# Optimization experiments

Hardware: AMD Instinct MI355X
Metric: run time of the kernel (lower is better)

The kernel has to match this reference:

```python
import jax, jax.numpy as jnp
import numpy as np

B, P, ED, AD, DD, E, V, T = 64, 196, 2048, 512, 512, 300, 1000, 96


def setup_inputs() -> dict:
    key = jax.random.key(0)
    ks = jax.random.split(key, 24)
    s = 0.02  # small init scale for weights
    lens = jax.random.randint(ks[2], (B,), 2, T + 1).astype(jnp.int32)
    lens = lens.at[0].set(T)  # ensure max(decode_lengths) == T-1 (static)
    return {
        'encoder_out': jax.random.normal(ks[0], (B, P, ED), jnp.float32),
        'encoded_captions': jax.random.randint(ks[1], (B, T), 0, V),
        'caption_lengths': lens,
        'emb': jax.random.uniform(ks[3], (V, E), jnp.float32, -0.1, 0.1),
        'W_enc_att': jax.random.normal(ks[4], (ED, AD), jnp.float32) * s,
        'b_enc_att': jnp.zeros((AD,), jnp.float32),
        'W_dec_att': jax.random.normal(ks[5], (DD, AD), jnp.float32) * s,
        'b_dec_att': jnp.zeros((AD,), jnp.float32),
        'w_full': jax.random.normal(ks[6], (AD,), jnp.float32) * s,
        'b_full': jnp.zeros((), jnp.float32),
        'W_init_h': jax.random.normal(ks[7], (ED, DD), jnp.float32) * s,
        'b_init_h': jnp.zeros((DD,), jnp.float32),
        'W_init_c': jax.random.normal(ks[8], (ED, DD), jnp.float32) * s,
        'b_init_c': jnp.zeros((DD,), jnp.float32),
        'W_fbeta': jax.random.normal(ks[9], (DD, ED), jnp.float32) * s,
        'b_fbeta': jnp.zeros((ED,), jnp.float32),
        'W_ih': jax.random.normal(ks[10], (E + ED, 4 * DD), jnp.float32) * s,
        'b_ih': jnp.zeros((4 * DD,), jnp.float32),
        'W_hh': jax.random.normal(ks[11], (DD, 4 * DD), jnp.float32) * s,
        'b_hh': jnp.zeros((4 * DD,), jnp.float32),
        'W_fc': jax.random.uniform(ks[12], (DD, V), jnp.float32, -0.1, 0.1),
        'b_fc': jnp.zeros((V,), jnp.float32),
    }


def reference(encoder_out, encoded_captions, caption_lengths, emb,
              W_enc_att, b_enc_att, W_dec_att, b_dec_att, w_full, b_full,
              W_init_h, b_init_h, W_init_c, b_init_c, W_fbeta, b_fbeta,
              W_ih, b_ih, W_hh, b_hh, W_fc, b_fc):
    # Sort by caption length, descending (stable like torch.sort on ints)
    sort_ind = jnp.argsort(-caption_lengths)
    lens = caption_lengths[sort_ind]
    eo = encoder_out[sort_ind]                  # [B,P,ED]
    caps = encoded_captions[sort_ind]           # [B,T]
    decode_lengths = lens - 1                   # [B]

    embs = emb[caps]                            # [B,T,E]
    mean_eo = eo.mean(axis=1)                   # [B,ED]
    h0 = mean_eo @ W_init_h + b_init_h          # [B,DD]
    c0 = mean_eo @ W_init_c + b_init_c

    # encoder-side attention projection is step-invariant: hoist it
    att1 = eo @ W_enc_att + b_enc_att           # [B,P,AD]

    Tdec = T - 1
    ts = jnp.arange(Tdec)
    masks = (decode_lengths[None, :] > ts[:, None]).astype(eo.dtype)  # [Tdec,B]
    emb_seq = jnp.swapaxes(embs[:, :Tdec, :], 0, 1)                    # [Tdec,B,E]

    def step(carry, xs):
        h, c = carry
        emb_t, m = xs                           # [B,E], [B]
        mb = m[:, None]
        # Bahdanau attention
        att2 = h @ W_dec_att + b_dec_att        # [B,AD]
        e = jnp.einsum('bpa,a->bp', jax.nn.relu(att1 + att2[:, None, :]), w_full) + b_full
        alpha = jax.nn.softmax(e, axis=1)       # [B,P]
        awe = jnp.einsum('bpd,bp->bd', eo, alpha)  # [B,ED]
        gate = jax.nn.sigmoid(h @ W_fbeta + b_fbeta)
        x = jnp.concatenate([emb_t, gate * awe], axis=1)  # [B,E+ED]
        # LSTMCell (torch gate order: i, f, g, o)
        gates = x @ W_ih + b_ih + h @ W_hh + b_hh
        i, f, g, o = jnp.split(gates, 4, axis=1)
        c_new = jax.nn.sigmoid(f) * c + jax.nn.sigmoid(i) * jnp.tanh(g)
        h_new = jax.nn.sigmoid(o) * jnp.tanh(c_new)
        # only active rows (sorted so they are a prefix) update state
        h2 = mb * h_new + (1.0 - mb) * h
        c2 = mb * c_new + (1.0 - mb) * c
        preds = (h2 @ W_fc + b_fc) * mb         # dropout = identity (eval)
        return (h2, c2), (preds, alpha * mb)

    (_, _), (preds, alphas) = jax.lax.scan(step, (h0, c0), (emb_seq, masks))
    predictions = jnp.swapaxes(preds, 0, 1)     # [B,Tdec,V]
    alphas = jnp.swapaxes(alphas, 0, 1)         # [B,Tdec,P]
    return predictions, caps, decode_lengths, alphas, sort_ind
```

## Files before the change

kernel.cpp:

```cpp
#include <hip/hip_runtime.h>
#include <stddef.h>
#include <math.h>

static constexpr int B = 64, P = 196, ED = 2048, AD = 512, DD = 512, E = 300, V = 1000, T = 96, TD = 95;
static constexpr int KX = E + ED;
static constexpr int KTOT = KX + DD;
static constexpr int KSPLIT = 8;
static constexpr int KPER = 368;
static constexpr int NG = 4 * DD;

static constexpr size_t POFF   = 0;
static constexpr size_t CAPOFF = (size_t)B * TD * V;
static constexpr size_t DLOFF  = CAPOFF + (size_t)B * T;
static constexpr size_t AOFF   = DLOFF + B;
static constexpr size_t SOFF   = AOFF + (size_t)B * TD * P;

__device__ __forceinline__ float sigm(float x) { return 1.0f / (1.0f + expf(-x)); }

__global__ __launch_bounds__(64) void k_sort(const int* __restrict__ lens,
                                             const int* __restrict__ caps_in,
                                             int* __restrict__ sidx,
                                             int* __restrict__ dlen,
                                             int* __restrict__ caps_s,
                                             float* __restrict__ out) {
    __shared__ int sl[B];
    __shared__ int ss[B];
    int i = threadIdx.x;
    sl[i] = lens[i];
    __syncthreads();
    int li = sl[i];
    int r = 0;
    for (int j = 0; j < B; j++) {
        int lj = sl[j];
        r += (lj > li) || (lj == li && j < i);
    }
    ss[r] = i;
    sidx[r] = i;
    dlen[r] = li - 1;
    out[DLOFF + r] = (float)(li - 1);
    out[SOFF + r] = (float)i;
    __syncthreads();
    for (int idx = i; idx < B * T; idx += B) {
        int b = idx / T, tt = idx % T;
        int v = caps_in[ss[b] * T + tt];
        caps_s[idx] = v;
        out[CAPOFF + idx] = (float)v;
    }
}

__global__ __launch_bounds__(256) void k_mean(const float* __restrict__ eo,
                                              const int* __restrict__ sidx,
                                              float* __restrict__ mean_eo) {
    int b = blockIdx.y;
    int d = blockIdx.x * 256 + threadIdx.x;
    const float* base = eo + ((size_t)sidx[b] * P) * ED + d;
    float s = 0.f;
    for (int p = 0; p < P; p++) s += base[(size_t)p * ED];
    mean_eo[(size_t)b * ED + d] = s * (1.0f / (float)P);
}

__global__ __launch_bounds__(256) void k_init(const float* __restrict__ mean_eo,
                                              const float* __restrict__ Wh, const float* __restrict__ bh,
                                              const float* __restrict__ Wc, const float* __restrict__ bc,
                                              float* __restrict__ h0, float* __restrict__ c0,
                                              float* __restrict__ xT) {
    int idx = blockIdx.x * 256 + threadIdx.x;
    int b = idx >> 9, j = idx & 511;
    const float* m = mean_eo + (size_t)b * ED;
    float ah = bh[j], ac = bc[j];
    for (int k = 0; k < ED; k++) {
        float mv = m[k];
        ah += mv * Wh[(size_t)k * DD + j];
        ac += mv * Wc[(size_t)k * DD + j];
    }
    h0[idx] = ah;
    c0[idx] = ac;
    xT[(size_t)(KX + j) * B + b] = ah;
}

__global__ __launch_bounds__(256) void k_att1(const float* __restrict__ eo,
                                              const float* __restrict__ W,
                                              const float* __restrict__ bias,
                                              const int* __restrict__ sidx,
                                              float* __restrict__ att1) {
    int m0 = blockIdx.x * 64, n0 = blockIdx.y * 64;
    __shared__ float sA[16][68];
    __shared__ float sB[16][68];
    int tid = threadIdx.x;
    int tx = tid & 15, ty = tid >> 4;
    float acc[4][4] = {};

    int la_m = tid >> 2;
    int la_k = (tid & 3) * 4;
    int lb_k = tid >> 4;
    int lb_n = (tid & 15) * 4;

    int mA = m0 + la_m;
    int bA = mA / P, pA = mA % P;
    const float* arow = eo + ((size_t)sidx[bA] * P + pA) * ED;

    for (int k0 = 0; k0 < ED; k0 += 16) {
        float4 av = *(const float4*)(arow + k0 + la_k);
        sA[la_k + 0][la_m] = av.x;
        sA[la_k + 1][la_m] = av.y;
        sA[la_k + 2][la_m] = av.z;
        sA[la_k + 3][la_m] = av.w;
        float4 bv = *(const float4*)(W + (size_t)(k0 + lb_k) * AD + n0 + lb_n);
        *(float4*)&sB[lb_k][lb_n] = bv;
        __syncthreads();
#pragma unroll
        for (int kk = 0; kk < 16; kk++) {
            float4 a4 = *(const float4*)&sA[kk][ty * 4];
            float4 b4 = *(const float4*)&sB[kk][tx * 4];
            float av_[4] = {a4.x, a4.y, a4.z, a4.w};
            float bv_[4] = {b4.x, b4.y, b4.z, b4.w};
#pragma unroll
            for (int i = 0; i < 4; i++)
#pragma unroll
                for (int j = 0; j < 4; j++) acc[i][j] += av_[i] * bv_[j];
        }
        __syncthreads();
    }
#pragma unroll
    for (int i = 0; i < 4; i++) {
        int m = m0 + ty * 4 + i;
        int n = n0 + tx * 4;
        float4 o;
        o.x = acc[i][0] + bias[n + 0];
        o.y = acc[i][1] + bias[n + 1];
        o.z = acc[i][2] + bias[n + 2];
        o.w = acc[i][3] + bias[n + 3];
        *(float4*)(att1 + (size_t)m * AD + n) = o;
    }
}

__global__ __launch_bounds__(256) void kA1(const float* __restrict__ hprev,
                                           const float* __restrict__ Wda, const float* __restrict__ bda,
                                           const float* __restrict__ Wfb, const float* __restrict__ bfb,
                                           const float* __restrict__ emb,
                                           const int* __restrict__ caps_s,
                                           float* __restrict__ att2g,
                                           float* __restrict__ fg,
                                           float* __restrict__ xT, int t) {
    int bx = blockIdx.x;
    int tid = threadIdx.x;
    if (bx >= 80) {
        int k0 = (bx - 80) * 60;
        for (int l = tid; l < 60 * 64; l += 256) {
            int r = l >> 6, b = l & 63;
            int k = k0 + r;
            int cap = caps_s[b * T + t];
            xT[(size_t)k * B + b] = emb[(size_t)cap * E + k];
        }
        return;
    }
    int n0 = bx * 32;
    bool is_att = (n0 < AD);
    __shared__ float sH[16][68];
    __shared__ float sW[16][36];
    float acc[4][2] = {};
    int tb = tid & 15, tn = tid >> 4;

    for (int k0 = 0; k0 < DD; k0 += 16) {
        {
            int b = tid >> 2, q = tid & 3;
            float4 hv = *(const float4*)(hprev + (size_t)b * DD + k0 + q * 4);
            sH[q * 4 + 0][b] = hv.x;
            sH[q * 4 + 1][b] = hv.y;
            sH[q * 4 + 2][b] = hv.z;
            sH[q * 4 + 3][b] = hv.w;
        }
        if (tid < 128) {
            int kk = tid >> 3, nn = (tid & 7) * 4;
            float4 wv;
            if (is_att) wv = *(const float4*)(Wda + (size_t)(k0 + kk) * AD + n0 + nn);
            else        wv = *(const float4*)(Wfb + (size_t)(k0 + kk) * ED + (n0 - AD) + nn);
            *(float4*)&sW[kk][nn] = wv;
        }
        __syncthreads();
#pragma unroll
        for (int kk = 0; kk < 16; kk++) {
            float4 hv = *(const float4*)&sH[kk][tb * 4];
            float w0 = sW[kk][tn * 2 + 0];
            float w1 = sW[kk][tn * 2 + 1];
            acc[0][0] += hv.x * w0; acc[0][1] += hv.x * w1;
            acc[1][0] += hv.y * w0; acc[1][1] += hv.y * w1;
            acc[2][0] += hv.z * w0; acc[2][1] += hv.z * w1;
            acc[3][0] += hv.w * w0; acc[3][1] += hv.w * w1;
        }
        __syncthreads();
    }
#pragma unroll
    for (int i = 0; i < 4; i++)
#pragma unroll
        for (int j = 0; j < 2; j++) {
            int b = tb * 4 + i;
            int n = n0 + tn * 2 + j;
            float v = acc[i][j];
            if (is_att) att2g[(size_t)b * AD + n] = v + bda[n];
            else {
                int d = n - AD;
                fg[(size_t)b * ED + d] = sigm(v + bfb[d]);
            }
        }
}

__global__ __launch_bounds__(1024) void kA2(const float* __restrict__ att2g,
                                            const float* __restrict__ att1,
                                            const float* __restrict__ wf,
                                            const float* __restrict__ bfv,
                                            const int* __restrict__ dlen,
                                            float* __restrict__ alpha,
                                            float* __restrict__ out, int t) {
    int b = blockIdx.x;
    int tid = threadIdx.x;
    __shared__ float sa2[AD];
    __shared__ float swf[AD];
    __shared__ float se[P];
    __shared__ float red[1024];

    if (tid < AD) {
        sa2[tid] = att2g[(size_t)b * AD + tid];
        swf[tid] = wf[tid];
    }
    __syncthreads();

    int w = tid >> 6, lane = tid & 63;
    float bf0 = bfv[0];
#pragma unroll 2
    for (int p = w; p < P; p += 16) {
        const float* row = att1 + ((size_t)b * P + p) * AD + lane * 8;
        float4 u0 = *(const float4*)row;
        float4 u1 = *(const float4*)(row + 4);
        float4 s0 = *(const float4*)&sa2[lane * 8];
        float4 s1 = *(const float4*)&sa2[lane * 8 + 4];
        float4 w0 = *(const float4*)&swf[lane * 8];
        float4 w1 = *(const float4*)&swf[lane * 8 + 4];
        float acc = fmaxf(u0.x + s0.x, 0.f) * w0.x + fmaxf(u0.y + s0.y, 0.f) * w0.y +
                    fmaxf(u0.z + s0.z, 0.f) * w0.z + fmaxf(u0.w + s0.w, 0.f) * w0.w +
                    fmaxf(u1.x + s1.x, 0.f) * w1.x + fmaxf(u1.y + s1.y, 0.f) * w1.y +
                    fmaxf(u1.z + s1.z, 0.f) * w1.z + fmaxf(u1.w + s1.w, 0.f) * w1.w;
#pragma unroll
        for (int m = 32; m >= 1; m >>= 1) acc += __shfl_xor(acc, m, 64);
        if (lane == 0) se[p] = acc + bf0;
    }
    __syncthreads();

    red[tid] = (tid < P) ? se[tid] : -1e30f;
    __syncthreads();
    for (int s = 512; s > 0; s >>= 1) {
        if (tid < s) red[tid] = fmaxf(red[tid], red[tid + s]);
        __syncthreads();
    }
    float mx = red[0];
    __syncthreads();
    float ex = (tid < P) ? expf(se[tid] - mx) : 0.f;
    red[tid] = ex;
    __syncthreads();
    for (int s = 512; s > 0; s >>= 1) {
        if (tid < s) red[tid] += red[tid + s];
        __syncthreads();
    }
    float inv = 1.0f / red[0];
    if (tid < P) {
        float a = ex * inv;
        alpha[(size_t)b * P + tid] = a;
        float m = (dlen[b] > t) ? 1.f : 0.f;
        out[AOFF + ((size_t)b * TD + t) * P + tid] = a * m;
    }
}

__global__ __launch_bounds__(256) void kB(const float* __restrict__ eo,
                                          const int* __restrict__ sidx,
                                          const float* __restrict__ alpha,
                                          const float* __restrict__ fg,
                                          float* __restrict__ xT) {
    int b = blockIdx.y, ch = blockIdx.x, tid = threadIdx.x;
    int pg = tid >> 6, lane = tid & 63;
    __shared__ float sal[P];
    __shared__ float part[4][260];
    if (tid < P) sal[tid] = alpha[(size_t)b * P + tid];
    __syncthreads();
    int d = ch * 256 + lane * 4;
    const float* base = eo + ((size_t)sidx[b] * P) * ED + d;
    float ax = 0.f, ay = 0.f, az = 0.f, aw = 0.f;
#pragma unroll 7
    for (int i = 0; i < 49; i++) {
        int p = pg + i * 4;
        float4 v = *(const float4*)(base + (size_t)p * ED);
        float a = sal[p];
        ax += v.x * a; ay += v.y * a; az += v.z * a; aw += v.w * a;
    }
    part[pg][lane * 4 + 0] = ax;
    part[pg][lane * 4 + 1] = ay;
    part[pg][lane * 4 + 2] = az;
    part[pg][lane * 4 + 3] = aw;
    __syncthreads();
    if (tid < 64) {
        int d0 = ch * 256 + tid * 4;
        float4 g = *(const float4*)(fg + (size_t)b * ED + d0);
        float s0 = part[0][tid * 4 + 0] + part[1][tid * 4 + 0] + part[2][tid * 4 + 0] + part[3][tid * 4 + 0];
        float s1 = part[0][tid * 4 + 1] + part[1][tid * 4 + 1] + part[2][tid * 4 + 1] + part[3][tid * 4 + 1];
        float s2 = part[0][tid * 4 + 2] + part[1][tid * 4 + 2] + part[2][tid * 4 + 2] + part[3][tid * 4 + 2];
        float s3 = part[0][tid * 4 + 3] + part[1][tid * 4 + 3] + part[2][tid * 4 + 3] + part[3][tid * 4 + 3];
        xT[(size_t)(E + d0 + 0) * B + b] = g.x * s0;
        xT[(size_t)(E + d0 + 1) * B + b] = g.y * s1;
        xT[(size_t)(E + d0 + 2) * B + b] = g.z * s2;
        xT[(size_t)(E + d0 + 3) * B + b] = g.w * s3;
    }
}

__global__ __launch_bounds__(256) void kC(const float* __restrict__ xT,
                                          const float* __restrict__ Wih,
                                          const float* __restrict__ Whh,
                                          float* __restrict__ part) {
    int bx = blockIdx.x;
    int ks = bx >> 6, nb = bx & 63;
    int n0 = nb * 32;
    int tid = threadIdx.x;
    int tb = tid & 15, tn = tid >> 4;
    __shared__ float sW[16][36];
    float acc[4][2] = {};
    int kbase = ks * KPER;

    for (int tile = 0; tile < 23; tile++) {
        int k0 = kbase + tile * 16;
        if (tid < 128) {
            int kk = tid >> 3, nn = (tid & 7) * 4;
            int kg = k0 + kk;
            float4 wv = make_float4(0.f, 0.f, 0.f, 0.f);
            if (kg < KX) wv = *(const float4*)&Wih[(size_t)kg * NG + n0 + nn];
            else if (kg < KTOT) wv = *(const float4*)&Whh[(size_t)(kg - KX) * NG + n0 + nn];
            *(float4*)&sW[kk][nn] = wv;
        }
        __syncthreads();
#pragma unroll
        for (int kk = 0; kk < 16; kk++) {
            int kg = k0 + kk;
            float4 xv = make_float4(0.f, 0.f, 0.f, 0.f);
            if (kg < KTOT) xv = *(const float4*)&xT[(size_t)kg * B + tb * 4];
            float w0 = sW[kk][tn * 2 + 0];
            float w1 = sW[kk][tn * 2 + 1];
            acc[0][0] += xv.x * w0; acc[0][1] += xv.x * w1;
            acc[1][0] += xv.y * w0; acc[1][1] += xv.y * w1;
            acc[2][0] += xv.z * w0; acc[2][1] += xv.z * w1;
            acc[3][0] += xv.w * w0; acc[3][1] += xv.w * w1;
        }
        __syncthreads();
    }
    float* pr = part + (size_t)ks * B * NG;
#pragma unroll
    for (int i = 0; i < 4; i++)
#pragma unroll
        for (int j = 0; j < 2; j++) {
            int b = tb * 4 + i, n = n0 + tn * 2 + j;
            pr[(size_t)b * NG + n] = acc[i][j];
        }
}

__global__ __launch_bounds__(256) void kD(const float* __restrict__ part,
                                          const float* __restrict__ bih,
                                          const float* __restrict__ bhh,
                                          const float* __restrict__ hprev,
                                          const float* __restrict__ cc,
                                          const int* __restrict__ dlen,
                                          float* __restrict__ hseq_t,
                                          float* __restrict__ cn,
                                          float* __restrict__ xT, int t) {
    int idx = blockIdx.x * 256 + threadIdx.x;
    int b = idx >> 9, j = idx & 511;
    float gi = bih[j] + bhh[j];
    float gf = bih[DD + j] + bhh[DD + j];
    float gg = bih[2 * DD + j] + bhh[2 * DD + j];
    float go = bih[3 * DD + j] + bhh[3 * DD + j];
#pragma unroll
    for (int s = 0; s < KSPLIT; s++) {
        const float* pr = part + ((size_t)s * B + b) * NG;
        gi += pr[j];
        gf += pr[DD + j];
        gg += pr[2 * DD + j];
        go += pr[3 * DD + j];
    }
    float cold = cc[idx], hold = hprev[idx];
    float cnew = sigm(gf) * cold + sigm(gi) * tanhf(gg);
    float hnew = sigm(go) * tanhf(cnew);
    bool m = dlen[b] > t;
    float h2 = m ? hnew : hold;
    float c2 = m ? cnew : cold;
    hseq_t[idx] = h2;
    cn[idx] = c2;
    xT[(size_t)(KX + j) * B + b] = h2;
}

__global__ __launch_bounds__(256) void k_predsall(const float* __restrict__ hseq,
                                                  const float* __restrict__ Wfc,
                                                  const float* __restrict__ bfc,
                                                  const int* __restrict__ dlen,
                                                  float* __restrict__ out) {
    int t = blockIdx.x;
    int n0 = blockIdx.y * 64;
    int tid = threadIdx.x;
    int tx = tid & 15, ty = tid >> 4;
    __shared__ float sA[16][68];
    __shared__ float sB[16][68];
    float acc[4][4] = {};
    const float* A = hseq + (size_t)t * B * DD;

    for (int k0 = 0; k0 < DD; k0 += 16) {
        {
            int b = tid >> 2, q = tid & 3;
            float4 hv = *(const float4*)(A + (size_t)b * DD + k0 + q * 4);
            sA[q * 4 + 0][b] = hv.x;
            sA[q * 4 + 1][b] = hv.y;
            sA[q * 4 + 2][b] = hv.z;
            sA[q * 4 + 3][b] = hv.w;
        }
        {
            int kk = tid >> 4, nn = (tid & 15) * 4;
            int c = n0 + nn;
            const float* wrow = Wfc + (size_t)(k0 + kk) * V;
            float4 wv;
            if (c + 3 < V) wv = *(const float4*)(wrow + c);
            else {
                wv.x = (c + 0 < V) ? wrow[c + 0] : 0.f;
                wv.y = (c + 1 < V) ? wrow[c + 1] : 0.f;
                wv.z = (c + 2 < V) ? wrow[c + 2] : 0.f;
                wv.w = (c + 3 < V) ? wrow[c + 3] : 0.f;
            }
            *(float4*)&sB[kk][nn] = wv;
        }
        __syncthreads();
#pragma unroll
        for (int kk = 0; kk < 16; kk++) {
            float4 a4 = *(const float4*)&sA[kk][ty * 4];
            float4 b4 = *(const float4*)&sB[kk][tx * 4];
            float av_[4] = {a4.x, a4.y, a4.z, a4.w};
            float bv_[4] = {b4.x, b4.y, b4.z, b4.w};
#pragma unroll
            for (int i = 0; i < 4; i++)
#pragma unroll
                for (int j = 0; j < 4; j++) acc[i][j] += av_[i] * bv_[j];
        }
        __syncthreads();
    }
#pragma unroll
    for (int i = 0; i < 4; i++) {
        int b = ty * 4 + i;
        bool m = dlen[b] > t;
#pragma unroll
        for (int j = 0; j < 4; j++) {
            int n = n0 + tx * 4 + j;
            if (n < V)
                out[POFF + ((size_t)b * TD + t) * V + n] = m ? (acc[i][j] + bfc[n]) : 0.f;
        }
    }
}

extern "C" void kernel_launch(void* const* d_in, const int* in_sizes, int n_in,
                              void* d_out, int out_size, void* d_ws, size_t ws_size,
                              hipStream_t stream) {
    const float* eo    = (const float*)d_in[0];
    const int*   caps  = (const int*)d_in[1];
    const int*   lens  = (const int*)d_in[2];
    const float* emb   = (const float*)d_in[3];
    const float* Wea   = (const float*)d_in[4];
    const float* bea   = (const float*)d_in[5];
    const float* Wda   = (const float*)d_in[6];
    const float* bda   = (const float*)d_in[7];
    const float* wfull = (const float*)d_in[8];
    const float* bfull = (const float*)d_in[9];
    const float* Wih_  = (const float*)d_in[10];
    const float* bih_  = (const float*)d_in[11];
    const float* Wic   = (const float*)d_in[12];
    const float* bic   = (const float*)d_in[13];
    const float* Wfb   = (const float*)d_in[14];
    const float* bfb   = (const float*)d_in[15];
    const float* Wih   = (const float*)d_in[16];
    const float* bih   = (const float*)d_in[17];
    const float* Whh   = (const float*)d_in[18];
    const float* bhh   = (const float*)d_in[19];
    const float* Wfc   = (const float*)d_in[20];
    const float* bfc   = (const float*)d_in[21];
    float* out = (float*)d_out;

    char* w = (char*)d_ws;
    auto carve = [&](size_t bytes) -> void* {
        void* p = (void*)w;
        w += (bytes + 255) & ~(size_t)255;
        return p;
    };
    int* sidx      = (int*)carve(B * 4);
    int* dlen      = (int*)carve(B * 4);
    int* caps_s    = (int*)carve((size_t)B * T * 4);
    float* mean_eo = (float*)carve((size_t)B * ED * 4);
    float* h0      = (float*)carve((size_t)B * DD * 4);
    float* cb0     = (float*)carve((size_t)B * DD * 4);
    float* cb1     = (float*)carve((size_t)B * DD * 4);
    float* att1    = (float*)carve((size_t)B * P * AD * 4);
    float* alphaW  = (float*)carve((size_t)B * P * 4);
    float* att2g   = (float*)carve((size_t)B * AD * 4);
    float* fg      = (float*)carve((size_t)B * ED * 4);
    float* xT      = (float*)carve((size_t)KTOT * B * 4);
    float* part    = (float*)carve((size_t)KSPLIT * B * NG * 4);
    float* hseq    = (float*)carve((size_t)TD * B * DD * 4);
    float* cb[2] = {cb0, cb1};

    k_sort<<<1, 64, 0, stream>>>(lens, caps, sidx, dlen, caps_s, out);
    k_mean<<<dim3(ED / 256, B), 256, 0, stream>>>(eo, sidx, mean_eo);
    k_init<<<(B * DD) / 256, 256, 0, stream>>>(mean_eo, Wih_, bih_, Wic, bic, h0, cb0, xT);
    k_att1<<<dim3((B * P) / 64, AD / 64), 256, 0, stream>>>(eo, Wea, bea, sidx, att1);

    for (int t = 0; t < TD; t++) {
        const float* hprev = (t == 0) ? h0 : (hseq + (size_t)(t - 1) * B * DD);
        float* cc = cb[t & 1];
        float* cn = cb[(t + 1) & 1];
        kA1<<<85, 256, 0, stream>>>(hprev, Wda, bda, Wfb, bfb, emb, caps_s, att2g, fg, xT, t);
        kA2<<<64, 1024, 0, stream>>>(att2g, att1, wfull, bfull, dlen, alphaW, out, t);
        kB<<<dim3(8, B), 256, 0, stream>>>(eo, sidx, alphaW, fg, xT);
        kC<<<512, 256, 0, stream>>>(xT, Wih, Whh, part);
        kD<<<(B * DD) / 256, 256, 0, stream>>>(part, bih, bhh, hprev, cc, dlen,
                                               hseq + (size_t)t * B * DD, cn, xT, t);
    }
    k_predsall<<<dim3(TD, 16), 256, 0, stream>>>(hseq, Wfc, bfc, dlen, out);
}
```

Measured before the change: 17.75 ms.

## Fuse LSTM cell update and attention projection into per-step kernels, precompute embeddings

Result: slower. 19.30 ms (+8.7%).

```diff
diff --git a/kernel.cpp b/kernel.cpp
--- a/kernel.cpp
+++ b/kernel.cpp
@@ -45,6 +45,19 @@
         int v = caps_in[ss[b] * T + tt];
         caps_s[idx] = v;
         out[CAPOFF + idx] = (float)v;
+    }
+}
+
+__global__ __launch_bounds__(256) void k_emball(const float* __restrict__ emb,
+                                                const int* __restrict__ caps_s,
+                                                float* __restrict__ embT) {
+    int t = blockIdx.x;
+    int k0 = blockIdx.y * 60;
+    for (int l = threadIdx.x; l < 60 * 64; l += 256) {
+        int r = l >> 6, b = l & 63;
+        int k = k0 + r;
+        int cap = caps_s[b * T + t];
+        embT[((size_t)t * E + k) * B + b] = emb[(size_t)cap * E + k];
     }
 }
 
@@ -134,95 +147,77 @@
     }
 }
 
-__global__ __launch_bounds__(256) void kA1(const float* __restrict__ hprev,
-                                           const float* __restrict__ Wda, const float* __restrict__ bda,
-                                           const float* __restrict__ Wfb, const float* __restrict__ bfb,
-                                           const float* __restrict__ emb,
-                                           const int* __restrict__ caps_s,
-                                           float* __restrict__ att2g,
-                                           float* __restrict__ fg,
-                                           float* __restrict__ xT, int t) {
-    int bx = blockIdx.x;
-    int tid = threadIdx.x;
-    if (bx >= 80) {
-        int k0 = (bx - 80) * 60;
-        for (int l = tid; l < 60 * 64; l += 256) {
-            int r = l >> 6, b = l & 63;
-            int k = k0 + r;
-            int cap = caps_s[b * T + t];
-            xT[(size_t)k * B + b] = emb[(size_t)cap * E + k];
-        }
-        return;
-    }
-    int n0 = bx * 32;
-    bool is_att = (n0 < AD);
-    __shared__ float sH[16][68];
-    __shared__ float sW[16][36];
-    float acc[4][2] = {};
-    int tb = tid & 15, tn = tid >> 4;
-
-    for (int k0 = 0; k0 < DD; k0 += 16) {
-        {
-            int b = tid >> 2, q = tid & 3;
-            float4 hv = *(const float4*)(hprev + (size_t)b * DD + k0 + q * 4);
-            sH[q * 4 + 0][b] = hv.x;
-            sH[q * 4 + 1][b] = hv.y;
-            sH[q * 4 + 2][b] = hv.z;
-            sH[q * 4 + 3][b] = hv.w;
-        }
-        if (tid < 128) {
-            int kk = tid >> 3, nn = (tid & 7) * 4;
-            float4 wv;
-            if (is_att) wv = *(const float4*)(Wda + (size_t)(k0 + kk) * AD + n0 + nn);
-            else        wv = *(const float4*)(Wfb + (size_t)(k0 + kk) * ED + (n0 - AD) + nn);
-            *(float4*)&sW[kk][nn] = wv;
-        }
-        __syncthreads();
-#pragma unroll
-        for (int kk = 0; kk < 16; kk++) {
-            float4 hv = *(const float4*)&sH[kk][tb * 4];
-            float w0 = sW[kk][tn * 2 + 0];
-            float w1 = sW[kk][tn * 2 + 1];
-            acc[0][0] += hv.x * w0; acc[0][1] += hv.x * w1;
-            acc[1][0] += hv.y * w0; acc[1][1] += hv.y * w1;
-            acc[2][0] += hv.z * w0; acc[2][1] += hv.z * w1;
-            acc[3][0] += hv.w * w0; acc[3][1] += hv.w * w1;
-        }
-        __syncthreads();
-    }
-#pragma unroll
-    for (int i = 0; i < 4; i++)
-#pragma unroll
-        for (int j = 0; j < 2; j++) {
-            int b = tb * 4 + i;
-            int n = n0 + tn * 2 + j;
-            float v = acc[i][j];
-            if (is_att) att2g[(size_t)b * AD + n] = v + bda[n];
-            else {
-                int d = n - AD;
-                fg[(size_t)b * ED + d] = sigm(v + bfb[d]);
-            }
-        }
-}
-
-__global__ __launch_bounds__(1024) void kA2(const float* __restrict__ att2g,
-                                            const float* __restrict__ att1,
-                                            const float* __restrict__ wf,
-                                            const float* __restrict__ bfv,
-                                            const int* __restrict__ dlen,
-                                            float* __restrict__ alpha,
-                                            float* __restrict__ out, int t) {
+__global__ __launch_bounds__(1024) void kA2f(const float* __restrict__ part,
+                                             const float* __restrict__ bih,
+                                             const float* __restrict__ bhh,
+                                             const float* __restrict__ h0,
+                                             const float* __restrict__ cread,
+                                             float* __restrict__ cwrite,
+                                             const float* __restrict__ Wda,
+                                             const float* __restrict__ bda,
+                                             const float* __restrict__ att1,
+                                             const float* __restrict__ wf,
+                                             const float* __restrict__ bfv,
+                                             const int* __restrict__ dlen,
+                                             float* __restrict__ alpha,
+                                             float* __restrict__ xT,
+                                             float* __restrict__ hseq,
+                                             float* __restrict__ out, int t) {
     int b = blockIdx.x;
     int tid = threadIdx.x;
+    __shared__ float sh[DD];
+    __shared__ float swf[AD];
     __shared__ float sa2[AD];
-    __shared__ float swf[AD];
+    __shared__ float pa[2][AD];
     __shared__ float se[P];
     __shared__ float red[1024];
 
-    if (tid < AD) {
-        sa2[tid] = att2g[(size_t)b * AD + tid];
-        swf[tid] = wf[tid];
-    }
+    if (tid >= 512) {
+        swf[tid - 512] = wf[tid - 512];
+    } else {
+        int j = tid;
+        if (t == 0) {
+            sh[j] = h0[(size_t)b * DD + j];
+        } else {
+            float gi = bih[j] + bhh[j];
+            float gf = bih[DD + j] + bhh[DD + j];
+            float gg = bih[2 * DD + j] + bhh[2 * DD + j];
+            float go = bih[3 * DD + j] + bhh[3 * DD + j];
+#pragma unroll
+            for (int s = 0; s < KSPLIT; s++) {
+                const float* pr = part + ((size_t)s * B + b) * NG;
+                gi += pr[j];
+                gf += pr[DD + j];
+                gg += pr[2 * DD + j];
+                go += pr[3 * DD + j];
+            }
+            const float* holds = (t == 1) ? h0 : (hseq + (size_t)(t - 2) * B * DD);
+            float cold = cread[(size_t)b * DD + j];
+            float hold = holds[(size_t)b * DD + j];
+            float cnew = sigm(gf) * cold + sigm(gi) * tanhf(gg);
+            float hnew = sigm(go) * tanhf(cnew);
+            bool m = dlen[b] > (t - 1);
+            float h2 = m ? hnew : hold;
+            float c2 = m ? cnew : cold;
+            sh[j] = h2;
+            hseq[(size_t)(t - 1) * B * DD + (size_t)b * DD + j] = h2;
+            cwrite[(size_t)b * DD + j] = c2;
+            xT[(size_t)(KX + j) * B + b] = h2;
+        }
+    }
+    __syncthreads();
+
+    {
+        int n = tid & 511, half = tid >> 9;
+        int kb = half * 256;
+        float acc = 0.f;
+#pragma unroll 8
+        for (int ki = 0; ki < 256; ki++)
+            acc += sh[kb + ki] * Wda[(size_t)(kb + ki) * AD + n];
+        pa[half][n] = acc;
+    }
+    __syncthreads();
+    if (tid < 512) sa2[tid] = pa[0][tid] + pa[1][tid] + bda[tid];
     __syncthreads();
 
     int w = tid >> 6, lane = tid & 63;
@@ -241,7 +236,7 @@
                     fmaxf(u1.x + s1.x, 0.f) * w1.x + fmaxf(u1.y + s1.y, 0.f) * w1.y +
                     fmaxf(u1.z + s1.z, 0.f) * w1.z + fmaxf(u1.w + s1.w, 0.f) * w1.w;
 #pragma unroll
-        for (int m = 32; m >= 1; m >>= 1) acc += __shfl_xor(acc, m, 64);
+        for (int mm = 32; mm >= 1; mm >>= 1) acc += __shfl_xor(acc, mm, 64);
         if (lane == 0) se[p] = acc + bf0;
     }
     __syncthreads();
@@ -270,19 +265,37 @@
     }
 }
 
-__global__ __launch_bounds__(256) void kB(const float* __restrict__ eo,
-                                          const int* __restrict__ sidx,
-                                          const float* __restrict__ alpha,
-                                          const float* __restrict__ fg,
-                                          float* __restrict__ xT) {
-    int b = blockIdx.y, ch = blockIdx.x, tid = threadIdx.x;
+__global__ __launch_bounds__(256) void kBf(const float* __restrict__ eo,
+                                           const int* __restrict__ sidx,
+                                           const float* __restrict__ hprev,
+                                           const float* __restrict__ Wfb,
+                                           const float* __restrict__ bfb,
+                                           const float* __restrict__ alpha,
+                                           float* __restrict__ xT) {
+    int bid = blockIdx.x;
+    int ch = bid & 7, b = bid >> 3;
+    int tid = threadIdx.x;
+    __shared__ float sh[DD];
+    __shared__ float sal[P];
+    __shared__ float sfg[256];
+    __shared__ float partl[4][260];
+
+    sh[tid] = hprev[(size_t)b * DD + tid];
+    sh[tid + 256] = hprev[(size_t)b * DD + tid + 256];
+    if (tid < P) sal[tid] = alpha[(size_t)b * P + tid];
+    __syncthreads();
+
+    {
+        int d = ch * 256 + tid;
+        float fgv = bfb[d];
+#pragma unroll 8
+        for (int k = 0; k < DD; k++) fgv += sh[k] * Wfb[(size_t)k * ED + d];
+        sfg[tid] = sigm(fgv);
+    }
+
     int pg = tid >> 6, lane = tid & 63;
-    __shared__ float sal[P];
-    __shared__ float part[4][260];
-    if (tid < P) sal[tid] = alpha[(size_t)b * P + tid];
-    __syncthreads();
-    int d = ch * 256 + lane * 4;
-    const float* base = eo + ((size_t)sidx[b] * P) * ED + d;
+    int d4 = ch * 256 + lane * 4;
+    const float* base = eo + ((size_t)sidx[b] * P) * ED + d4;
     float ax = 0.f, ay = 0.f, az = 0.f, aw = 0.f;
 #pragma unroll 7
     for (int i = 0; i < 49; i++) {
@@ -291,26 +304,26 @@
         float a = sal[p];
         ax += v.x * a; ay += v.y * a; az += v.z * a; aw += v.w * a;
     }
-    part[pg][lane * 4 + 0] = ax;
-    part[pg][lane * 4 + 1] = ay;
-    part[pg][lane * 4 + 2] = az;
-    part[pg][lane * 4 + 3] = aw;
+    partl[pg][lane * 4 + 0] = ax;
+    partl[pg][lane * 4 + 1] = ay;
+    partl[pg][lane * 4 + 2] = az;
+    partl[pg][lane * 4 + 3] = aw;
     __syncthreads();
     if (tid < 64) {
         int d0 = ch * 256 + tid * 4;
-        float4 g = *(const float4*)(fg + (size_t)b * ED + d0);
-        float s0 = part[0][tid * 4 + 0] + part[1][tid * 4 + 0] + part[2][tid * 4 + 0] + part[3][tid * 4 + 0];
-        float s1 = part[0][tid * 4 + 1] + part[1][tid * 4 + 1] + part[2][tid * 4 + 1] + part[3][tid * 4 + 1];
-        float s2 = part[0][tid * 4 + 2] + part[1][tid * 4 + 2] + part[2][tid * 4 + 2] + part[3][tid * 4 + 2];
-        float s3 = part[0][tid * 4 + 3] + part[1][tid * 4 + 3] + part[2][tid * 4 + 3] + part[3][tid * 4 + 3];
-        xT[(size_t)(E + d0 + 0) * B + b] = g.x * s0;
-        xT[(size_t)(E + d0 + 1) * B + b] = g.y * s1;
-        xT[(size_t)(E + d0 + 2) * B + b] = g.z * s2;
-        xT[(size_t)(E + d0 + 3) * B + b] = g.w * s3;
+        float s0 = partl[0][tid * 4 + 0] + partl[1][tid * 4 + 0] + partl[2][tid * 4 + 0] + partl[3][tid * 4 + 0];
+        float s1 = partl[0][tid * 4 + 1] + partl[1][tid * 4 + 1] + partl[2][tid * 4 + 1] + partl[3][tid * 4 + 1];
+        float s2 = partl[0][tid * 4 + 2] + partl[1][tid * 4 + 2] + partl[2][tid * 4 + 2] + partl[3][tid * 4 + 2];
+        float s3 = partl[0][tid * 4 + 3] + partl[1][tid * 4 + 3] + partl[2][tid * 4 + 3] + partl[3][tid * 4 + 3];
+        xT[(size_t)(E + d0 + 0) * B + b] = sfg[tid * 4 + 0] * s0;
+        xT[(size_t)(E + d0 + 1) * B + b] = sfg[tid * 4 + 1] * s1;
+        xT[(size_t)(E + d0 + 2) * B + b] = sfg[tid * 4 + 2] * s2;
+        xT[(size_t)(E + d0 + 3) * B + b] = sfg[tid * 4 + 3] * s3;
     }
 }
 
 __global__ __launch_bounds__(256) void kC(const float* __restrict__ xT,
+                                          const float* __restrict__ embT_t,
                                           const float* __restrict__ Wih,
                                           const float* __restrict__ Whh,
                                           float* __restrict__ part) {
@@ -338,7 +351,8 @@
         for (int kk = 0; kk < 16; kk++) {
             int kg = k0 + kk;
             float4 xv = make_float4(0.f, 0.f, 0.f, 0.f);
-            if (kg < KTOT) xv = *(const float4*)&xT[(size_t)kg * B + tb * 4];
+            if (kg < E) xv = *(const float4*)&embT_t[(size_t)kg * B + tb * 4];
+            else if (kg < KTOT) xv = *(const float4*)&xT[(size_t)kg * B + tb * 4];
             float w0 = sW[kk][tn * 2 + 0];
             float w1 = sW[kk][tn * 2 + 1];
             acc[0][0] += xv.x * w0; acc[0][1] += xv.x * w1;
@@ -366,7 +380,7 @@
                                           const int* __restrict__ dlen,
                                           float* __restrict__ hseq_t,
                                           float* __restrict__ cn,
-                                          float* __restrict__ xT, int t) {
+                                          int t) {
     int idx = blockIdx.x * 256 + threadIdx.x;
     int b = idx >> 9, j = idx & 511;
     float gi = bih[j] + bhh[j];
@@ -389,7 +403,6 @@
     float c2 = m ? cnew : cold;
     hseq_t[idx] = h2;
     cn[idx] = c2;
-    xT[(size_t)(KX + j) * B + b] = h2;
 }
 
 __global__ __launch_bounds__(256) void k_predsall(const float* __restrict__ hseq,
@@ -498,28 +511,29 @@
     float* cb1     = (float*)carve((size_t)B * DD * 4);
     float* att1    = (float*)carve((size_t)B * P * AD * 4);
     float* alphaW  = (float*)carve((size_t)B * P * 4);
-    float* att2g   = (float*)carve((size_t)B * AD * 4);
-    float* fg      = (float*)carve((size_t)B * ED * 4);
     float* xT      = (float*)carve((size_t)KTOT * B * 4);
     float* part    = (float*)carve((size_t)KSPLIT * B * NG * 4);
     float* hseq    = (float*)carve((size_t)TD * B * DD * 4);
-    float* cb[2] = {cb0, cb1};
+    float* embT    = (float*)carve((size_t)TD * E * B * 4);
 
     k_sort<<<1, 64, 0, stream>>>(lens, caps, sidx, dlen, caps_s, out);
+    k_emball<<<dim3(TD, 5), 256, 0, stream>>>(emb, caps_s, embT);
     k_mean<<<dim3(ED / 256, B), 256, 0, stream>>>(eo, sidx, mean_eo);
-    k_init<<<(B * DD) / 256, 256, 0, stream>>>(mean_eo, Wih_, bih_, Wic, bic, h0, cb0, xT);
+    k_init<<<(B * DD) / 256, 256, 0, stream>>>(mean_eo, Wih_, bih_, Wic, bic, h0, cb1, xT);
     k_att1<<<dim3((B * P) / 64, AD / 64), 256, 0, stream>>>(eo, Wea, bea, sidx, att1);
 
     for (int t = 0; t < TD; t++) {
+        const float* cread  = (t & 1) ? cb1 : cb0;
+        float*       cwrite = (t & 1) ? cb0 : cb1;
+        kA2f<<<64, 1024, 0, stream>>>(part, bih, bhh, h0, cread, cwrite,
+                                      Wda, bda, att1, wfull, bfull, dlen,
+                                      alphaW, xT, hseq, out, t);
         const float* hprev = (t == 0) ? h0 : (hseq + (size_t)(t - 1) * B * DD);
-        float* cc = cb[t & 1];
-        float* cn = cb[(t + 1) & 1];
-        kA1<<<85, 256, 0, stream>>>(hprev, Wda, bda, Wfb, bfb, emb, caps_s, att2g, fg, xT, t);
-        kA2<<<64, 1024, 0, stream>>>(att2g, att1, wfull, bfull, dlen, alphaW, out, t);
-        kB<<<dim3(8, B), 256, 0, stream>>>(eo, sidx, alphaW, fg, xT);
-        kC<<<512, 256, 0, stream>>>(xT, Wih, Whh, part);
-        kD<<<(B * DD) / 256, 256, 0, stream>>>(part, bih, bhh, hprev, cc, dlen,
-                                               hseq + (size_t)t * B * DD, cn, xT, t);
-    }
+        kBf<<<512, 256, 0, stream>>>(eo, sidx, hprev, Wfb, bfb, alphaW, xT);
+        kC<<<512, 256, 0, stream>>>(xT, embT + (size_t)t * E * B, Wih, Whh, part);
+    }
+    kD<<<(B * DD) / 256, 256, 0, stream>>>(part, bih, bhh,
+                                           hseq + (size_t)(TD - 2) * B * DD, cb1, dlen,
+                                           hseq + (size_t)(TD - 1) * B * DD, cb0, TD - 1);
     k_predsall<<<dim3(TD, 16), 256, 0, stream>>>(hseq, Wfc, bfc, dlen, out);
 }
```
